# Performance work log

Measured on AMD Instinct MI355X. Metric: run time of the kernel, lower is better.

## Reference

```python
import jax, jax.numpy as jnp
import numpy as np

IMG = 640.0  # square input image, strides 16/32 -> 40x40 and 20x20 grids

def _decode_level(raw, stride):
    # raw: [B, 5+C, H, W] -> [B, H*W, 5+C] with xy/wh decoded (get_output_and_grid)
    b, ch, h, w = raw.shape
    out = raw.transpose(0, 2, 3, 1).reshape(b, h * w, ch)
    yv, xv = jnp.meshgrid(jnp.arange(h), jnp.arange(w), indexing='ij')
    gx = xv.reshape(-1).astype(raw.dtype)
    gy = yv.reshape(-1).astype(raw.dtype)
    xy = (out[..., :2] + jnp.stack([gx, gy], -1)[None]) * stride
    wh = jnp.exp(out[..., 2:4]) * stride
    out = jnp.concatenate([xy, wh, out[..., 4:]], -1)
    return out, gx, gy, jnp.full((h * w,), stride, raw.dtype)

def _pairwise_iou(a, b):
    # a:[M,4], b:[A,4] in cxcywh -> [M,A] (bboxes_iou, xyxy=False)
    tl = jnp.maximum(a[:, None, :2] - a[:, None, 2:] * 0.5, b[None, :, :2] - b[None, :, 2:] * 0.5)
    br = jnp.minimum(a[:, None, :2] + a[:, None, 2:] * 0.5, b[None, :, :2] + b[None, :, 2:] * 0.5)
    inter = jnp.prod(br - tl, -1) * (tl < br).all(-1)
    area_a = a[:, 2] * a[:, 3]
    area_b = b[:, 2] * b[:, 3]
    return inter / (area_a[:, None] + area_b[None, :] - inter + 1e-16)

def _iou_loss(p, t):
    # YOLOX IOUloss (loss_type='iou'): 1 - iou^2, elementwise over [..., 4] cxcywh
    tl = jnp.maximum(p[..., :2] - p[..., 2:] * 0.5, t[..., :2] - t[..., 2:] * 0.5)
    br = jnp.minimum(p[..., :2] + p[..., 2:] * 0.5, t[..., :2] + t[..., 2:] * 0.5)
    inter = jnp.prod(br - tl, -1) * (tl < br).all(-1)
    iou = inter / (p[..., 2] * p[..., 3] + t[..., 2] * t[..., 3] - inter + 1e-16)
    return 1.0 - iou ** 2

def _bce_logits(x, t):
    # BCEWithLogitsLoss(reduction='none') = softplus(x) - x*t (stable)
    return jnp.logaddexp(0.0, x) - x * t

def _assign_one(bbox_p, cls_p, obj_p, gtb, gtc, gtv, ax, ay, st):
    # SimOTA assignment for one image (mask form of get_assignments, which is @no_grad).
    # bbox_p:[A,4] cls_p:[A,C] obj_p:[A] gtb:[M,4] px cxcywh, gtv:[M] valid mask.
    m = gtb.shape[0]
    axc = (ax + 0.5) * st
    ayc = (ay + 0.5) * st
    gl = gtb[:, 0] - 0.5 * gtb[:, 2]; gr = gtb[:, 0] + 0.5 * gtb[:, 2]
    gtp = gtb[:, 1] - 0.5 * gtb[:, 3]; gbt = gtb[:, 1] + 0.5 * gtb[:, 3]
    in_box = ((axc[None] > gl[:, None]) & (axc[None] < gr[:, None]) &
              (ayc[None] > gtp[:, None]) & (ayc[None] < gbt[:, None])) & gtv[:, None]
    r = 2.5  # center_radius
    in_ctr = ((axc[None] > gtb[:, 0:1] - r * st[None]) & (axc[None] < gtb[:, 0:1] + r * st[None]) &
              (ayc[None] > gtb[:, 1:2] - r * st[None]) & (ayc[None] < gtb[:, 1:2] + r * st[None])) & gtv[:, None]
    fg_cand = (in_box | in_ctr).any(0)          # candidate anchors (fg_mask pre-filter)
    in_both = in_box & in_ctr
    ious = _pairwise_iou(gtb, bbox_p)            # [M,A]
    p = jnp.sqrt(jax.nn.sigmoid(cls_p) * jax.nn.sigmoid(obj_p)[:, None])[None]  # [1,A,C]
    t = jax.nn.one_hot(gtc, cls_p.shape[-1], dtype=p.dtype)[:, None, :]          # [M,1,C]
    eps = 1e-12
    cls_cost = -(t * jnp.log(p + eps) + (1.0 - t) * jnp.log(1.0 - p + eps)).sum(-1)
    invalid = (~fg_cand)[None] | (~gtv)[:, None]
    cost = cls_cost - 3.0 * jnp.log(ious + 1e-8) + 1e5 * (~in_both) + 1e9 * invalid
    ious_m = jnp.where(invalid, 0.0, ious)
    topk, _ = jax.lax.top_k(ious_m, 10)
    dk = jnp.maximum(topk.sum(-1).astype(jnp.int32), 1)  # dynamic_k, clamp min=1
    dk = jnp.where(gtv, dk, 0)
    ranks = jnp.argsort(jnp.argsort(cost, axis=1), axis=1)
    matching = ranks < dk[:, None]                        # top dynamic_k lowest-cost anchors per gt
    conflict = matching.sum(0) > 1
    best_gt = jnp.argmin(cost, 0)
    matching = jnp.where(conflict[None], jnp.arange(m)[:, None] == best_gt[None], matching)
    fg = matching.any(0)
    matched = jnp.argmax(matching, 0).astype(jnp.int32)
    pred_iou = jnp.where(matching, ious, 0.0).sum(0)
    return fg, matched, pred_iou

def _forward(out_l0, out_l1, gt_boxes, gt_classes, num_gts):
    ncls = out_l0.shape[1] - 5
    decs, xs, ys, ss = [], [], [], []
    for raw, stride in ((out_l0, 16.0), (out_l1, 32.0)):
        d, gx, gy, s = _decode_level(raw, stride)
        decs.append(d); xs.append(gx); ys.append(gy); ss.append(s)
    outputs = jnp.concatenate(decs, 1)  # [B, A, 5+C]
    ax = jnp.concatenate(xs); ay = jnp.concatenate(ys); st = jnp.concatenate(ss)
    bbox_p = outputs[..., :4]; obj_p = outputs[..., 4]; cls_p = outputs[..., 5:]
    gtb = gt_boxes * IMG  # normalized -> pixels (imgs_w == imgs_h == IMG)
    gtv = jnp.arange(gt_boxes.shape[1])[None, :] < num_gts[:, None]
    sg = jax.lax.stop_gradient  # get_assignments runs under torch.no_grad
    fg, matched, pred_iou = jax.vmap(_assign_one, in_axes=(0, 0, 0, 0, 0, 0, None, None, None))(
        sg(bbox_p), sg(cls_p), sg(obj_p), sg(gtb), gt_classes, gtv, ax, ay, st)
    fgf = fg.astype(outputs.dtype)
    cls_t = jax.nn.one_hot(jnp.take_along_axis(gt_classes, matched, 1), ncls,
                           dtype=outputs.dtype) * pred_iou[..., None] * fgf[..., None]
    reg_t = jnp.take_along_axis(gtb, matched[..., None], 1)  # [B,A,4]
    num_fg = jnp.maximum(fgf.sum(), 1.0)
    loss_iou = (_iou_loss(bbox_p, reg_t) * fgf).sum() / num_fg
    loss_obj = _bce_logits(obj_p, fgf).sum() / num_fg
    loss_cls = (_bce_logits(cls_p, cls_t) * fgf[..., None]).sum() / num_fg
    total = 5.0 * loss_iou + loss_obj + loss_cls
    return (total, 5.0 * loss_iou, loss_obj, loss_cls,
            num_fg / jnp.maximum(num_gts.sum().astype(outputs.dtype), 1.0))

def setup_inputs() -> dict:
    key = jax.random.key(0)
    k1, k2, k3, k4, k5 = jax.random.split(key, 5)
    return {
        'out_l0': jax.random.normal(k1, (64, 25, 40, 40), jnp.float32),
        'out_l1': jax.random.normal(k2, (64, 25, 20, 20), jnp.float32),
        'gt_boxes': jax.random.uniform(k3, (64, 100, 4), jnp.float32, 1e-3, 1.0),
        'gt_classes': jax.random.randint(k4, (64, 100), 0, 20).astype(jnp.int32),
        'num_gts': jax.random.randint(k5, (64,), 0, 100).astype(jnp.int32),
    }

def reference(out_l0, out_l1, gt_boxes, gt_classes, num_gts):
    return _forward(out_l0, out_l1, gt_boxes, gt_classes, num_gts)
```

## Files before the change

kernel.cpp:

```cpp
#include <hip/hip_runtime.h>
#include <cfloat>
#include <climits>

#define NB 64
#define NA 2000
#define NAP 2048
#define NA0 1600
#define NC 20
#define NM 100

__device__ __forceinline__ void anchor_geom(int a, float& axc, float& ayc, float& st) {
    if (a < NA0) {
        st = 16.0f;
        int x = a % 40, y = a / 40;
        axc = ((float)x + 0.5f) * 16.0f;
        ayc = ((float)y + 0.5f) * 16.0f;
    } else {
        st = 32.0f;
        int aa = a - NA0;
        int x = aa % 20, y = aa / 20;
        axc = ((float)x + 0.5f) * 32.0f;
        ayc = ((float)y + 0.5f) * 32.0f;
    }
}

__device__ __forceinline__ float cost_pair(const float4 g, float clsc, const float4 pb,
                                           float axc, float ayc, float st, bool fc) {
    float tlx = fmaxf(g.x - 0.5f * g.z, pb.x - 0.5f * pb.z);
    float tly = fmaxf(g.y - 0.5f * g.w, pb.y - 0.5f * pb.w);
    float brx = fminf(g.x + 0.5f * g.z, pb.x + 0.5f * pb.z);
    float bry = fminf(g.y + 0.5f * g.w, pb.y + 0.5f * pb.w);
    float inter = (brx - tlx) * (bry - tly);
    bool ok = (tlx < brx) && (tly < bry);
    inter = ok ? inter : 0.0f;
    float iou = inter / ((g.z * g.w + pb.z * pb.w) - inter + 1e-16f);
    bool ib = (axc > g.x - 0.5f * g.z) && (axc < g.x + 0.5f * g.z)
           && (ayc > g.y - 0.5f * g.w) && (ayc < g.y + 0.5f * g.w);
    bool ic = (axc > g.x - 2.5f * st) && (axc < g.x + 2.5f * st)
           && (ayc > g.y - 2.5f * st) && (ayc < g.y + 2.5f * st);
    return ((clsc - 3.0f * __logf(iou + 1e-8f)) + ((ib && ic) ? 0.0f : 1e5f)) + (fc ? 0.0f : 1e9f);
}

__device__ __forceinline__ unsigned int wave_max_u32(unsigned int x) {
    unsigned int y;
    y = (unsigned)__builtin_amdgcn_update_dpp((int)x, (int)x, 0x111, 0xf, 0xf, false); x = max(x, y);
    y = (unsigned)__builtin_amdgcn_update_dpp((int)x, (int)x, 0x112, 0xf, 0xf, false); x = max(x, y);
    y = (unsigned)__builtin_amdgcn_update_dpp((int)x, (int)x, 0x114, 0xf, 0xf, false); x = max(x, y);
    y = (unsigned)__builtin_amdgcn_update_dpp((int)x, (int)x, 0x118, 0xf, 0xf, false); x = max(x, y);
    y = (unsigned)__builtin_amdgcn_update_dpp((int)x, (int)x, 0x142, 0xa, 0xf, false); x = max(x, y);
    y = (unsigned)__builtin_amdgcn_update_dpp((int)x, (int)x, 0x143, 0xc, 0xf, false); x = max(x, y);
    return (unsigned)__builtin_amdgcn_readlane((int)x, 63);
}
__device__ __forceinline__ unsigned int wave_min_u32(unsigned int x) {
    unsigned int y;
    y = (unsigned)__builtin_amdgcn_update_dpp((int)x, (int)x, 0x111, 0xf, 0xf, false); x = min(x, y);
    y = (unsigned)__builtin_amdgcn_update_dpp((int)x, (int)x, 0x112, 0xf, 0xf, false); x = min(x, y);
    y = (unsigned)__builtin_amdgcn_update_dpp((int)x, (int)x, 0x114, 0xf, 0xf, false); x = min(x, y);
    y = (unsigned)__builtin_amdgcn_update_dpp((int)x, (int)x, 0x118, 0xf, 0xf, false); x = min(x, y);
    y = (unsigned)__builtin_amdgcn_update_dpp((int)x, (int)x, 0x142, 0xa, 0xf, false); x = min(x, y);
    y = (unsigned)__builtin_amdgcn_update_dpp((int)x, (int)x, 0x143, 0xc, 0xf, false); x = min(x, y);
    return (unsigned)__builtin_amdgcn_readlane((int)x, 63);
}

__global__ __launch_bounds__(256) void k_decode(const float* __restrict__ l0, const float* __restrict__ l1,
                                                const float* __restrict__ gt_boxes, const int* __restrict__ num_gts,
                                                float4* __restrict__ dec, float* __restrict__ qq,
                                                unsigned long long* __restrict__ fgw, unsigned int* __restrict__ cm) {
    int b = blockIdx.y;
    int a = blockIdx.x * 256 + threadIdx.x;
    int lane = threadIdx.x & 63;
    __shared__ float4 sext[NM];
    __shared__ float2 sctr[NM];
    __shared__ int sng;
    if (threadIdx.x < NM) {
        float4 g = ((const float4*)gt_boxes)[b * NM + threadIdx.x];
        g.x *= 640.0f; g.y *= 640.0f; g.z *= 640.0f; g.w *= 640.0f;
        sext[threadIdx.x] = make_float4(g.x - 0.5f * g.z, g.x + 0.5f * g.z,
                                        g.y - 0.5f * g.w, g.y + 0.5f * g.w);
        sctr[threadIdx.x] = make_float2(g.x, g.y);
    }
    if (threadIdx.x == 0) sng = num_gts[b];
    __syncthreads();

    bool real = a < NA;
    size_t pidx = (size_t)b * NAP + a;

    if (!real) {
        dec[pidx] = make_float4(0.f, 0.f, 0.f, 0.f);
#pragma unroll
        for (int c = 0; c < NC; c++) qq[((size_t)b * NC + c) * NAP + a] = 0.0f;
        cm[pidx] = 0;
        unsigned long long mk = __ballot(0);
        if (lane == 0) fgw[(size_t)b * 32 + (a >> 6)] = mk;
        return;
    }

    float v[25];
    if (a < NA0) {
        const float* p = l0 + (size_t)b * 25 * NA0 + a;
#pragma unroll
        for (int c = 0; c < 25; c++) v[c] = p[(size_t)c * NA0];
    } else {
        const float* p = l1 + (size_t)b * 25 * 400 + (a - NA0);
#pragma unroll
        for (int c = 0; c < 25; c++) v[c] = p[(size_t)c * 400];
    }
    float axc, ayc, st;
    anchor_geom(a, axc, ayc, st);
    float gx, gy;
    if (a < NA0) { gx = (float)(a % 40); gy = (float)(a / 40); }
    else { int aa = a - NA0; gx = (float)(aa % 20); gy = (float)(aa / 20); }
    float4 pb;
    pb.x = (v[0] + gx) * st;
    pb.y = (v[1] + gy) * st;
    pb.z = expf(v[2]) * st;
    pb.w = expf(v[3]) * st;
    dec[pidx] = pb;

    float sob = 1.0f / (1.0f + __expf(-v[4]));
    float d[NC];
    float s = 0.0f;
#pragma unroll
    for (int c = 0; c < NC; c++) {
        float sc = 1.0f / (1.0f + __expf(-v[5 + c]));
        float p = sqrtf(sc * sob);
        float lp = __logf(p + 1e-12f);
        float lq = __logf(1.0f - p + 1e-12f);
        s += -lq;
        d[c] = lq - lp;
    }
#pragma unroll
    for (int c = 0; c < NC; c++)
        qq[((size_t)b * NC + c) * NAP + a] = s + d[c];

    int ng = sng;
    int f = 0;
    float rst = 2.5f * st;
    for (int m = 0; m < ng; m++) {
        float4 e = sext[m];
        float2 cc = sctr[m];
        bool ib = (axc > e.x) && (axc < e.y) && (ayc > e.z) && (ayc < e.w);
        bool ic = (axc > cc.x - rst) && (axc < cc.x + rst) && (ayc > cc.y - rst) && (ayc < cc.y + rst);
        if (ib || ic) { f = 1; break; }
    }
    unsigned long long mk = __ballot(f);
    if (lane == 0) fgw[(size_t)b * 32 + (a >> 6)] = mk;
    cm[pidx] = 0;
}

__global__ __launch_bounds__(256) void k_assign(const float* __restrict__ gt_boxes, const int* __restrict__ gt_classes,
                                                const int* __restrict__ num_gts, const float4* __restrict__ dec,
                                                const float* __restrict__ qq, const unsigned long long* __restrict__ fgw,
                                                unsigned int* __restrict__ cm) {
    int wave = threadIdx.x >> 6;
    int lane = threadIdx.x & 63;
    int row = __builtin_amdgcn_readfirstlane(blockIdx.x * 4 + wave);
    int b = row / NM, m = row - b * NM;
    if (m >= num_gts[b]) return;

    float4 g = ((const float4*)gt_boxes)[b * NM + m];
    g.x *= 640.0f; g.y *= 640.0f; g.z *= 640.0f; g.w *= 640.0f;
    int tc = gt_classes[b * NM + m];
    const float* qrow = qq + ((size_t)b * NC + tc) * NAP;
    size_t bNA = (size_t)b * NAP;

    float glx = g.x - 0.5f * g.z, grx = g.x + 0.5f * g.z;
    float gty = g.y - 0.5f * g.w, gby = g.y + 0.5f * g.w;
    float areag = g.z * g.w;
    float c16l = g.x - 40.0f, c16r = g.x + 40.0f, c16t = g.y - 40.0f, c16b = g.y + 40.0f;
    float c32l = g.x - 80.0f, c32r = g.x + 80.0f, c32t = g.y - 80.0f, c32b = g.y + 80.0f;

    unsigned int ik[32], ck[32];
#pragma unroll
    for (int j = 0; j < 32; j++) {
        int a = j * 64 + lane;
        float stj = (j < 25) ? 16.0f : 32.0f;
        int rel = (j < 25) ? a : (a - NA0);
        int W = (j < 25) ? 40 : 20;
        int gyv = rel / W;
        int gxv = rel - gyv * W;
        float axc = ((float)gxv + 0.5f) * stj;
        float ayc = ((float)gyv + 0.5f) * stj;
        unsigned long long fw = fgw[(size_t)b * 32 + j];
        bool fc = (fw >> lane) & 1ULL;
        float4 pb = dec[bNA + a];
        float clsc = qrow[a];
        float tlx = fmaxf(glx, pb.x - 0.5f * pb.z);
        float tly = fmaxf(gty, pb.y - 0.5f * pb.w);
        float brx = fminf(grx, pb.x + 0.5f * pb.z);
        float bry = fminf(gby, pb.y + 0.5f * pb.w);
        float inter = (brx - tlx) * (bry - tly);
        bool ok = (tlx < brx) && (tly < bry);
        inter = ok ? inter : 0.0f;
        float iou = inter / ((areag + pb.z * pb.w) - inter + 1e-16f);
        bool ib = (axc > glx) && (axc < grx) && (ayc > gty) && (ayc < gby);
        bool ic = (j < 25) ? ((axc > c16l) && (axc < c16r) && (ayc > c16t) && (ayc < c16b))
                           : ((axc > c32l) && (axc < c32r) && (ayc > c32t) && (ayc < c32b));
        float cc = ((clsc - 3.0f * __logf(iou + 1e-8f)) + ((ib && ic) ? 0.0f : 1e5f)) + (fc ? 0.0f : 1e9f);
        float im = fc ? iou : 0.0f;
        ik[j] = (__float_as_uint(im) & 0xFFFFF800u) | (unsigned)a;
        ck[j] = (__float_as_uint(cc) & 0xFFFFF800u) | (unsigned)a;
    }

    float s10 = 0.0f;
#pragma unroll 1
    for (int k = 0; k < 10; k++) {
        unsigned int t[16];
#pragma unroll
        for (int h = 0; h < 16; h++) t[h] = max(ik[2 * h], ik[2 * h + 1]);
#pragma unroll
        for (int w = 8; w >= 1; w >>= 1)
#pragma unroll
            for (int h = 0; h < w; h++) t[h] = max(t[h], t[h + w]);
        unsigned int mx = wave_max_u32(t[0]);
        if ((mx & 0xFFFFF800u) == 0u) break;
        s10 += __uint_as_float(mx & 0xFFFFF800u);
#pragma unroll
        for (int j = 0; j < 32; j++) ik[j] = (ik[j] == mx) ? 0u : ik[j];
    }
    int dk = __builtin_amdgcn_readfirstlane((int)s10);
    if (dk < 1) dk = 1;

    unsigned int mb = 0;
#pragma unroll 1
    for (int k = 0; k < dk; k++) {
        unsigned int t[16];
#pragma unroll
        for (int h = 0; h < 16; h++) t[h] = min(ck[2 * h], ck[2 * h + 1]);
#pragma unroll
        for (int w = 8; w >= 1; w >>= 1)
#pragma unroll
            for (int h = 0; h < w; h++) t[h] = min(t[h], t[h + w]);
        unsigned int mn = wave_min_u32(t[0]);
#pragma unroll
        for (int j = 0; j < 32; j++) {
            bool e = (ck[j] == mn);
            mb |= e ? (1u << j) : 0u;
            ck[j] = e ? 0xFFFFFFFFu : ck[j];
        }
    }

    unsigned int inc = (1u << 20) + (unsigned)m;
#pragma unroll
    for (int j = 0; j < 32; j++) {
        if ((mb >> j) & 1u) atomicAdd(&cm[bNA + j * 64 + lane], inc);
    }
}

__global__ __launch_bounds__(256) void k_conflict(const float* __restrict__ gt_boxes, const int* __restrict__ gt_classes,
                                                  const int* __restrict__ num_gts, const float4* __restrict__ dec,
                                                  const float* __restrict__ qq, const unsigned long long* __restrict__ fgw,
                                                  unsigned int* __restrict__ cm) {
    int gtid = blockIdx.x * 256 + threadIdx.x;
    int lane = threadIdx.x & 63;
    int base = gtid & ~63;
    unsigned int word = cm[gtid];
    unsigned long long msk = __ballot((word >> 20) >= 2u);
    if (msk == 0ull) return;
    int b = base >> 11;
    int ng = num_gts[b];
    while (msk) {
        int t = __ffsll((long long)msk) - 1;
        msk &= msk - 1;
        int idx = base + t;
        int a = idx & (NAP - 1);
        float4 pb = dec[idx];
        float axc, ayc, st;
        anchor_geom(a, axc, ayc, st);
        bool fc = (fgw[(size_t)b * 32 + (a >> 6)] >> (a & 63)) & 1ULL;
        unsigned int best = 0xFFFFFFFFu;
#pragma unroll
        for (int half = 0; half < 2; half++) {
            int m = half * 64 + lane;
            if (m < ng) {
                float4 g = ((const float4*)gt_boxes)[b * NM + m];
                g.x *= 640.0f; g.y *= 640.0f; g.z *= 640.0f; g.w *= 640.0f;
                int tcm = gt_classes[b * NM + m];
                float clsc = qq[((size_t)b * NC + tcm) * NAP + a];
                float cc = cost_pair(g, clsc, pb, axc, ayc, st, fc);
                unsigned int key = (__float_as_uint(cc) & 0xFFFFF800u) | (unsigned)m;
                best = min(best, key);
            }
        }
#pragma unroll
        for (int o = 1; o < 64; o <<= 1) {
            unsigned int ov = (unsigned int)__shfl_xor((int)best, o);
            best = min(best, ov);
        }
        if (lane == 0) cm[idx] = (1u << 20) | (best & 0x7FFu);
    }
}

__global__ __launch_bounds__(256) void k_resolve(const float* __restrict__ l0, const float* __restrict__ l1,
                                                 const float* __restrict__ gt_boxes, const int* __restrict__ gt_classes,
                                                 const float4* __restrict__ dec,
                                                 const unsigned int* __restrict__ cm,
                                                 float* __restrict__ partials) {
    int idx = blockIdx.x * 256 + threadIdx.x;
    int b = idx / NA, a = idx - b * NA;
    size_t pidx = (size_t)b * NAP + a;

    float objv;
    if (a < NA0) objv = l0[((size_t)b * 25 + 4) * NA0 + a];
    else         objv = l1[((size_t)b * 25 + 4) * 400 + (a - NA0)];

    unsigned int word = cm[pidx];
    bool fg = (word >> 20) > 0;
    float fgf = fg ? 1.0f : 0.0f;
    float lobj = (fmaxf(objv, 0.0f) + log1pf(expf(-fabsf(objv)))) - objv * fgf;
    float liou = 0.0f, lcls = 0.0f;

    if (fg) {
        float4 pb = dec[pidx];
        int m = (int)(word & 0xFFFFFu);
        float4 g = ((const float4*)gt_boxes)[b * NM + m];
        g.x *= 640.0f; g.y *= 640.0f; g.z *= 640.0f; g.w *= 640.0f;
        float tlx = fmaxf(pb.x - 0.5f * pb.z, g.x - 0.5f * g.z);
        float tly = fmaxf(pb.y - 0.5f * pb.w, g.y - 0.5f * g.w);
        float brx = fminf(pb.x + 0.5f * pb.z, g.x + 0.5f * g.z);
        float bry = fminf(pb.y + 0.5f * pb.w, g.y + 0.5f * g.w);
        float inter = (brx - tlx) * (bry - tly);
        bool ok = (tlx < brx) && (tly < bry);
        inter = ok ? inter : 0.0f;
        float iou = inter / ((pb.z * pb.w + g.z * g.w) - inter + 1e-16f);
        liou = 1.0f - iou * iou;
        float piou = iou;
        int tcm = gt_classes[b * NM + m];
#pragma unroll
        for (int c2 = 0; c2 < NC; c2++) {
            float x;
            if (a < NA0) x = l0[((size_t)b * 25 + 5 + c2) * NA0 + a];
            else         x = l1[((size_t)b * 25 + 5 + c2) * 400 + (a - NA0)];
            float t = (c2 == tcm) ? piou : 0.0f;
            lcls += (fmaxf(x, 0.0f) + log1pf(expf(-fabsf(x)))) - x * t;
        }
    }

    __shared__ float s0[256], s1[256], s2[256], s3[256];
    int t = threadIdx.x;
    s0[t] = lobj; s1[t] = liou; s2[t] = lcls; s3[t] = fgf;
    __syncthreads();
    for (int o = 128; o > 0; o >>= 1) {
        if (t < o) { s0[t] += s0[t + o]; s1[t] += s1[t + o]; s2[t] += s2[t + o]; s3[t] += s3[t + o]; }
        __syncthreads();
    }
    if (t == 0) {
        partials[blockIdx.x * 4 + 0] = s0[0];
        partials[blockIdx.x * 4 + 1] = s1[0];
        partials[blockIdx.x * 4 + 2] = s2[0];
        partials[blockIdx.x * 4 + 3] = s3[0];
    }
}

__global__ __launch_bounds__(256) void k_final(const float* __restrict__ partials, int nblocks,
                                               const int* __restrict__ num_gts, float* __restrict__ out) {
    __shared__ float s0[256], s1[256], s2[256], s3[256];
    int t = threadIdx.x;
    float a0 = 0, a1 = 0, a2 = 0, a3 = 0;
    for (int i = t; i < nblocks; i += 256) {
        a0 += partials[i * 4 + 0];
        a1 += partials[i * 4 + 1];
        a2 += partials[i * 4 + 2];
        a3 += partials[i * 4 + 3];
    }
    s0[t] = a0; s1[t] = a1; s2[t] = a2; s3[t] = a3;
    __syncthreads();
    for (int o = 128; o > 0; o >>= 1) {
        if (t < o) { s0[t] += s0[t + o]; s1[t] += s1[t + o]; s2[t] += s2[t + o]; s3[t] += s3[t + o]; }
        __syncthreads();
    }
    if (t == 0) {
        int sg = 0;
        for (int i = 0; i < NB; i++) sg += num_gts[i];
        float num_fg = fmaxf(s3[0], 1.0f);
        float li5 = 5.0f * (s1[0] / num_fg);
        float lo = s0[0] / num_fg;
        float lcx = s2[0] / num_fg;
        out[0] = li5 + lo + lcx;
        out[1] = li5;
        out[2] = lo;
        out[3] = lcx;
        out[4] = num_fg / fmaxf((float)sg, 1.0f);
    }
}

extern "C" void kernel_launch(void* const* d_in, const int* in_sizes, int n_in,
                              void* d_out, int out_size, void* d_ws, size_t ws_size,
                              hipStream_t stream) {
    const float* l0 = (const float*)d_in[0];
    const float* l1 = (const float*)d_in[1];
    const float* gt_boxes = (const float*)d_in[2];
    const int* gt_classes = (const int*)d_in[3];
    const int* num_gts = (const int*)d_in[4];
    float* out = (float*)d_out;

    char* w = (char*)d_ws;
    float4* dec = (float4*)(w);
    float* qq   = (float*)(w + 2097152);
    unsigned long long* fgw = (unsigned long long*)(w + 12582912);
    unsigned int* cm = (unsigned int*)(w + 12599296);
    float* partials = (float*)(w + 13123584);

    (void)n_in; (void)in_sizes; (void)out_size; (void)ws_size;

    k_decode<<<dim3(8, NB), 256, 0, stream>>>(l0, l1, gt_boxes, num_gts, dec, qq, fgw, cm);
    k_assign<<<(NB * NM) / 4, 256, 0, stream>>>(gt_boxes, gt_classes, num_gts, dec, qq, fgw, cm);
    k_conflict<<<(NB * NAP) / 256, 256, 0, stream>>>(gt_boxes, gt_classes, num_gts, dec, qq, fgw, cm);
    k_resolve<<<(NB * NA) / 256, 256, 0, stream>>>(l0, l1, gt_boxes, gt_classes, dec, cm, partials);
    k_final<<<1, 256, 0, stream>>>(partials, (NB * NA) / 256, num_gts, out);
}
```

Measured before the change: 77.40 us.

## Split SimOTA assignment rows across two waves and precompute softplus class sums

Each GT row's assignment now runs on two waves, each holding 16 anchor chunks instead of 32. The per-half top-10 IoU values and top-k costs are merged through shared memory and a single lane, and selection uses a threshold. This halves the per-wave register arrays and serial reduction depth, at the cost of extra block barriers and a serial merge. Separately, the decode kernel precomputes the per-anchor sum of softplus over class logits, so the resolve kernel reads one logit instead of twenty and skips the transcendentals.

Result: faster. 73.57 us (-5.0%).

```diff
diff --git a/kernel.cpp b/kernel.cpp
--- a/kernel.cpp
+++ b/kernel.cpp
@@ -65,7 +65,8 @@
 __global__ __launch_bounds__(256) void k_decode(const float* __restrict__ l0, const float* __restrict__ l1,
                                                 const float* __restrict__ gt_boxes, const int* __restrict__ num_gts,
                                                 float4* __restrict__ dec, float* __restrict__ qq,
-                                                unsigned long long* __restrict__ fgw, unsigned int* __restrict__ cm) {
+                                                unsigned long long* __restrict__ fgw, unsigned int* __restrict__ cm,
+                                                float* __restrict__ sp) {
     int b = blockIdx.y;
     int a = blockIdx.x * 256 + threadIdx.x;
     int lane = threadIdx.x & 63;
@@ -90,6 +91,7 @@
 #pragma unroll
         for (int c = 0; c < NC; c++) qq[((size_t)b * NC + c) * NAP + a] = 0.0f;
         cm[pidx] = 0;
+        sp[pidx] = 0.0f;
         unsigned long long mk = __ballot(0);
         if (lane == 0) fgw[(size_t)b * 32 + (a >> 6)] = mk;
         return;
@@ -120,18 +122,22 @@
     float sob = 1.0f / (1.0f + __expf(-v[4]));
     float d[NC];
     float s = 0.0f;
+    float spv = 0.0f;
 #pragma unroll
     for (int c = 0; c < NC; c++) {
-        float sc = 1.0f / (1.0f + __expf(-v[5 + c]));
+        float x = v[5 + c];
+        float sc = 1.0f / (1.0f + __expf(-x));
         float p = sqrtf(sc * sob);
         float lp = __logf(p + 1e-12f);
         float lq = __logf(1.0f - p + 1e-12f);
         s += -lq;
         d[c] = lq - lp;
+        spv += fmaxf(x, 0.0f) + log1pf(__expf(-fabsf(x)));
     }
 #pragma unroll
     for (int c = 0; c < NC; c++)
         qq[((size_t)b * NC + c) * NAP + a] = s + d[c];
+    sp[pidx] = spv;
 
     int ng = sng;
     int f = 0;
@@ -152,98 +158,152 @@
                                                 const int* __restrict__ num_gts, const float4* __restrict__ dec,
                                                 const float* __restrict__ qq, const unsigned long long* __restrict__ fgw,
                                                 unsigned int* __restrict__ cm) {
-    int wave = threadIdx.x >> 6;
     int lane = threadIdx.x & 63;
-    int row = __builtin_amdgcn_readfirstlane(blockIdx.x * 4 + wave);
+    int wv = __builtin_amdgcn_readfirstlane((int)(threadIdx.x >> 6));
+    int rloc = wv >> 1, half = wv & 1;
+    int row = __builtin_amdgcn_readfirstlane((int)(blockIdx.x * 2 + rloc));
     int b = row / NM, m = row - b * NM;
-    if (m >= num_gts[b]) return;
-
-    float4 g = ((const float4*)gt_boxes)[b * NM + m];
-    g.x *= 640.0f; g.y *= 640.0f; g.z *= 640.0f; g.w *= 640.0f;
-    int tc = gt_classes[b * NM + m];
-    const float* qrow = qq + ((size_t)b * NC + tc) * NAP;
+    bool valid = (m < num_gts[b]);
+
+    __shared__ unsigned int lA[2][2][10];
+    __shared__ unsigned int lB[2][2][10];
+    __shared__ unsigned int lmeta[2];
+    __shared__ unsigned int lthr[2];
+
+    unsigned int ik[16], ck[16];
     size_t bNA = (size_t)b * NAP;
-
-    float glx = g.x - 0.5f * g.z, grx = g.x + 0.5f * g.z;
-    float gty = g.y - 0.5f * g.w, gby = g.y + 0.5f * g.w;
-    float areag = g.z * g.w;
-    float c16l = g.x - 40.0f, c16r = g.x + 40.0f, c16t = g.y - 40.0f, c16b = g.y + 40.0f;
-    float c32l = g.x - 80.0f, c32r = g.x + 80.0f, c32t = g.y - 80.0f, c32b = g.y + 80.0f;
-
-    unsigned int ik[32], ck[32];
-#pragma unroll
-    for (int j = 0; j < 32; j++) {
-        int a = j * 64 + lane;
-        float stj = (j < 25) ? 16.0f : 32.0f;
-        int rel = (j < 25) ? a : (a - NA0);
-        int W = (j < 25) ? 40 : 20;
-        int gyv = rel / W;
-        int gxv = rel - gyv * W;
-        float axc = ((float)gxv + 0.5f) * stj;
-        float ayc = ((float)gyv + 0.5f) * stj;
-        unsigned long long fw = fgw[(size_t)b * 32 + j];
-        bool fc = (fw >> lane) & 1ULL;
-        float4 pb = dec[bNA + a];
-        float clsc = qrow[a];
-        float tlx = fmaxf(glx, pb.x - 0.5f * pb.z);
-        float tly = fmaxf(gty, pb.y - 0.5f * pb.w);
-        float brx = fminf(grx, pb.x + 0.5f * pb.z);
-        float bry = fminf(gby, pb.y + 0.5f * pb.w);
-        float inter = (brx - tlx) * (bry - tly);
-        bool ok = (tlx < brx) && (tly < bry);
-        inter = ok ? inter : 0.0f;
-        float iou = inter / ((areag + pb.z * pb.w) - inter + 1e-16f);
-        bool ib = (axc > glx) && (axc < grx) && (ayc > gty) && (ayc < gby);
-        bool ic = (j < 25) ? ((axc > c16l) && (axc < c16r) && (ayc > c16t) && (ayc < c16b))
+    unsigned int inc = (1u << 20) + (unsigned)m;
+
+    if (valid) {
+        float4 g = ((const float4*)gt_boxes)[b * NM + m];
+        g.x *= 640.0f; g.y *= 640.0f; g.z *= 640.0f; g.w *= 640.0f;
+        int tc = gt_classes[b * NM + m];
+        const float* qrow = qq + ((size_t)b * NC + tc) * NAP;
+
+        float glx = g.x - 0.5f * g.z, grx = g.x + 0.5f * g.z;
+        float gty = g.y - 0.5f * g.w, gby = g.y + 0.5f * g.w;
+        float areag = g.z * g.w;
+        float c16l = g.x - 40.0f, c16r = g.x + 40.0f, c16t = g.y - 40.0f, c16b = g.y + 40.0f;
+        float c32l = g.x - 80.0f, c32r = g.x + 80.0f, c32t = g.y - 80.0f, c32b = g.y + 80.0f;
+
+#pragma unroll
+        for (int j = 0; j < 16; j++) {
+            int jj = half * 16 + j;
+            int a = jj * 64 + lane;
+            bool lvl0 = jj < 25;
+            float stj = lvl0 ? 16.0f : 32.0f;
+            int rel = lvl0 ? a : (a - NA0);
+            int W = lvl0 ? 40 : 20;
+            int gyv = rel / W;
+            int gxv = rel - gyv * W;
+            float axc = ((float)gxv + 0.5f) * stj;
+            float ayc = ((float)gyv + 0.5f) * stj;
+            unsigned long long fw = fgw[(size_t)b * 32 + jj];
+            bool fc = (fw >> lane) & 1ULL;
+            float4 pb = dec[bNA + a];
+            float clsc = qrow[a];
+            float tlx = fmaxf(glx, pb.x - 0.5f * pb.z);
+            float tly = fmaxf(gty, pb.y - 0.5f * pb.w);
+            float brx = fminf(grx, pb.x + 0.5f * pb.z);
+            float bry = fminf(gby, pb.y + 0.5f * pb.w);
+            float inter = (brx - tlx) * (bry - tly);
+            bool ok = (tlx < brx) && (tly < bry);
+            inter = ok ? inter : 0.0f;
+            float iou = inter / ((areag + pb.z * pb.w) - inter + 1e-16f);
+            bool ib = (axc > glx) && (axc < grx) && (ayc > gty) && (ayc < gby);
+            bool ic = lvl0 ? ((axc > c16l) && (axc < c16r) && (ayc > c16t) && (ayc < c16b))
                            : ((axc > c32l) && (axc < c32r) && (ayc > c32t) && (ayc < c32b));
-        float cc = ((clsc - 3.0f * __logf(iou + 1e-8f)) + ((ib && ic) ? 0.0f : 1e5f)) + (fc ? 0.0f : 1e9f);
-        float im = fc ? iou : 0.0f;
-        ik[j] = (__float_as_uint(im) & 0xFFFFF800u) | (unsigned)a;
-        ck[j] = (__float_as_uint(cc) & 0xFFFFF800u) | (unsigned)a;
-    }
-
-    float s10 = 0.0f;
+            float cc = ((clsc - 3.0f * __logf(iou + 1e-8f)) + ((ib && ic) ? 0.0f : 1e5f)) + (fc ? 0.0f : 1e9f);
+            float im = fc ? iou : 0.0f;
+            ik[j] = (__float_as_uint(im) & 0xFFFFF800u) | (unsigned)a;
+            ck[j] = (__float_as_uint(cc) & 0xFFFFF800u) | (unsigned)a;
+        }
+
+        int k = 0;
 #pragma unroll 1
-    for (int k = 0; k < 10; k++) {
-        unsigned int t[16];
-#pragma unroll
-        for (int h = 0; h < 16; h++) t[h] = max(ik[2 * h], ik[2 * h + 1]);
-#pragma unroll
-        for (int w = 8; w >= 1; w >>= 1)
-#pragma unroll
-            for (int h = 0; h < w; h++) t[h] = max(t[h], t[h + w]);
-        unsigned int mx = wave_max_u32(t[0]);
-        if ((mx & 0xFFFFF800u) == 0u) break;
-        s10 += __uint_as_float(mx & 0xFFFFF800u);
-#pragma unroll
-        for (int j = 0; j < 32; j++) ik[j] = (ik[j] == mx) ? 0u : ik[j];
-    }
-    int dk = __builtin_amdgcn_readfirstlane((int)s10);
-    if (dk < 1) dk = 1;
-
-    unsigned int mb = 0;
+        for (; k < 10; ++k) {
+            unsigned int t[8];
+#pragma unroll
+            for (int h = 0; h < 8; h++) t[h] = max(ik[2 * h], ik[2 * h + 1]);
+#pragma unroll
+            for (int w = 4; w >= 1; w >>= 1)
+#pragma unroll
+                for (int h = 0; h < w; h++) t[h] = max(t[h], t[h + w]);
+            unsigned int mx = wave_max_u32(t[0]);
+            if ((mx & 0xFFFFF800u) == 0u) break;
+            if (lane == 0) lA[rloc][half][k] = mx;
+#pragma unroll
+            for (int j = 0; j < 16; j++) ik[j] = (ik[j] == mx) ? 0u : ik[j];
+        }
 #pragma unroll 1
-    for (int k = 0; k < dk; k++) {
-        unsigned int t[16];
-#pragma unroll
-        for (int h = 0; h < 16; h++) t[h] = min(ck[2 * h], ck[2 * h + 1]);
-#pragma unroll
-        for (int w = 8; w >= 1; w >>= 1)
-#pragma unroll
-            for (int h = 0; h < w; h++) t[h] = min(t[h], t[h + w]);
-        unsigned int mn = wave_min_u32(t[0]);
-#pragma unroll
-        for (int j = 0; j < 32; j++) {
-            bool e = (ck[j] == mn);
-            mb |= e ? (1u << j) : 0u;
-            ck[j] = e ? 0xFFFFFFFFu : ck[j];
-        }
-    }
-
-    unsigned int inc = (1u << 20) + (unsigned)m;
-#pragma unroll
-    for (int j = 0; j < 32; j++) {
-        if ((mb >> j) & 1u) atomicAdd(&cm[bNA + j * 64 + lane], inc);
+        for (; k < 10; ++k) if (lane == 0) lA[rloc][half][k] = 0u;
+    }
+    __syncthreads();
+
+    if (valid && half == 0 && lane == 0) {
+        int i0 = 0, i1 = 0;
+        float s = 0.0f;
+        for (int k = 0; k < 10; k++) {
+            unsigned int a0 = lA[rloc][0][i0], a1 = lA[rloc][1][i1];
+            unsigned int mx;
+            if (a1 > a0) { mx = a1; i1++; } else { mx = a0; i0++; }
+            s += __uint_as_float(mx & 0xFFFFF800u);
+        }
+        int dk = (int)s;
+        if (dk < 1) dk = 1;
+        lmeta[rloc] = (unsigned)dk;
+    }
+    __syncthreads();
+
+    int dkv = 0;
+    if (valid) dkv = __builtin_amdgcn_readfirstlane((int)lmeta[rloc]);
+
+    if (valid) {
+#pragma unroll 1
+        for (int k = 0; k < dkv; k++) {
+            unsigned int t[8];
+#pragma unroll
+            for (int h = 0; h < 8; h++) t[h] = min(ck[2 * h], ck[2 * h + 1]);
+#pragma unroll
+            for (int w = 4; w >= 1; w >>= 1)
+#pragma unroll
+                for (int h = 0; h < w; h++) t[h] = min(t[h], t[h + w]);
+            unsigned int mn = wave_min_u32(t[0]);
+            if (lane == 0) lB[rloc][half][k] = mn;
+#pragma unroll
+            for (int j = 0; j < 16; j++) ck[j] = (ck[j] == mn) ? 0xFFFFFFFFu : ck[j];
+        }
+    }
+    __syncthreads();
+
+    if (valid && half == 0 && lane == 0) {
+        int i0 = 0, i1 = 0;
+        unsigned int thr = 0;
+        for (int k = 0; k < dkv; k++) {
+            unsigned int a0 = lB[rloc][0][i0], a1 = lB[rloc][1][i1];
+            if (a1 < a0) { thr = a1; i1++; } else { thr = a0; i0++; }
+        }
+        lthr[rloc] = thr;
+    }
+    __syncthreads();
+
+    if (valid) {
+        unsigned int thr = (unsigned)__builtin_amdgcn_readfirstlane((int)lthr[rloc]);
+        unsigned int mb = 0;
+#pragma unroll
+        for (int j = 0; j < 16; j++) if (ck[j] <= thr) mb |= 1u << j;
+#pragma unroll 1
+        for (int k = 0; k < dkv; k++) {
+            unsigned int e = lB[rloc][half][k];
+            if (e <= thr) {
+                unsigned int idx = e & 0x7FFu;
+                if ((int)(idx & 63u) == lane) mb |= 1u << ((int)(idx >> 6) - half * 16);
+            }
+        }
+#pragma unroll
+        for (int j = 0; j < 16; j++) {
+            if ((mb >> j) & 1u) atomicAdd(&cm[bNA + (size_t)(half * 16 + j) * 64 + lane], inc);
+        }
     }
 }
 
@@ -295,6 +355,7 @@
                                                  const float* __restrict__ gt_boxes, const int* __restrict__ gt_classes,
                                                  const float4* __restrict__ dec,
                                                  const unsigned int* __restrict__ cm,
+                                                 const float* __restrict__ sp,
                                                  float* __restrict__ partials) {
     int idx = blockIdx.x * 256 + threadIdx.x;
     int b = idx / NA, a = idx - b * NA;
@@ -326,14 +387,10 @@
         liou = 1.0f - iou * iou;
         float piou = iou;
         int tcm = gt_classes[b * NM + m];
-#pragma unroll
-        for (int c2 = 0; c2 < NC; c2++) {
-            float x;
-            if (a < NA0) x = l0[((size_t)b * 25 + 5 + c2) * NA0 + a];
-            else         x = l1[((size_t)b * 25 + 5 + c2) * 400 + (a - NA0)];
-            float t = (c2 == tcm) ? piou : 0.0f;
-            lcls += (fmaxf(x, 0.0f) + log1pf(expf(-fabsf(x)))) - x * t;
-        }
+        float x_t;
+        if (a < NA0) x_t = l0[((size_t)b * 25 + 5 + tcm) * NA0 + a];
+        else         x_t = l1[((size_t)b * 25 + 5 + tcm) * 400 + (a - NA0)];
+        lcls = sp[pidx] - x_t * piou;
     }
 
     __shared__ float s0[256], s1[256], s2[256], s3[256];
@@ -399,13 +456,14 @@
     float* qq   = (float*)(w + 2097152);
     unsigned long long* fgw = (unsigned long long*)(w + 12582912);
     unsigned int* cm = (unsigned int*)(w + 12599296);
-    float* partials = (float*)(w + 13123584);
+    float* sp   = (float*)(w + 13123584);
+    float* partials = (float*)(w + 13647872);
 
     (void)n_in; (void)in_sizes; (void)out_size; (void)ws_size;
 
-    k_decode<<<dim3(8, NB), 256, 0, stream>>>(l0, l1, gt_boxes, num_gts, dec, qq, fgw, cm);
-    k_assign<<<(NB * NM) / 4, 256, 0, stream>>>(gt_boxes, gt_classes, num_gts, dec, qq, fgw, cm);
+    k_decode<<<dim3(8, NB), 256, 0, stream>>>(l0, l1, gt_boxes, num_gts, dec, qq, fgw, cm, sp);
+    k_assign<<<(NB * NM) / 2, 256, 0, stream>>>(gt_boxes, gt_classes, num_gts, dec, qq, fgw, cm);
     k_conflict<<<(NB * NAP) / 256, 256, 0, stream>>>(gt_boxes, gt_classes, num_gts, dec, qq, fgw, cm);
-    k_resolve<<<(NB * NA) / 256, 256, 0, stream>>>(l0, l1, gt_boxes, gt_classes, dec, cm, partials);
+    k_resolve<<<(NB * NA) / 256, 256, 0, stream>>>(l0, l1, gt_boxes, gt_classes, dec, cm, sp, partials);
     k_final<<<1, 256, 0, stream>>>(partials, (NB * NA) / 256, num_gts, out);
 }
```
